# Performance work log

Measured on AMD Instinct MI355X. Metric: run time of the kernel, lower is better.

Reference implementation:

```python
import jax, jax.numpy as jnp
import numpy as np

B, N, K, D_IN, D, L = 8, 8192, 6, 3, 256, 5
EPS_LN = 1e-5


def layernorm(x, g, b):
    m = jnp.mean(x, axis=-1, keepdims=True)
    v = jnp.mean((x - m) ** 2, axis=-1, keepdims=True)
    return (x - m) * jax.lax.rsqrt(v + EPS_LN) * g + b


def spmm_mean(v, knn):
    # sparse adj matmul: out[j] = sum_{n: j in knn[n]} v[n], then / k
    n, k = knn.shape[-2], knn.shape[-1]
    src = jnp.repeat(jnp.arange(n), k)  # [N*K]

    def one(vb, kb):
        return jnp.zeros_like(vb).at[kb.reshape(-1)].add(vb[src])

    return jax.vmap(one)(v, knn) / (k + 1e-6)


def grf_layer(h, knn, qkv_w, out_w, out_b, hops=3):
    q, k, v = jnp.split(h @ qkv_w, 3, axis=-1)
    for _ in range(hops):
        v = spmm_mean(v, knn)
        k = spmm_mean(k, knn)
    attn = jnp.sum(q * k, axis=-1, keepdims=True)
    return (attn * v) @ out_w + out_b


def linear_attention(h, qkv_w, out_w, out_b):
    q, k, v = jnp.split(h @ qkv_w, 3, axis=-1)
    q = jax.nn.relu(q) + 1e-6
    k = jax.nn.relu(k) + 1e-6
    kv = jnp.einsum('bnd,bne->bde', k, v)
    z = 1.0 / (jnp.einsum('bnd,bd->bn', q, k.sum(axis=1)) + 1e-6)
    attn = jnp.einsum('bnd,bde,bn->bne', q, kv, z)
    return attn @ out_w + out_b


def setup_inputs() -> dict:
    key = jax.random.key(0)
    ks = jax.random.split(key, 12)
    s = 0.02
    return {
        'x': jax.random.normal(ks[0], (B, N, D_IN), jnp.float32),
        'knn': jax.random.randint(ks[1], (B, N, K), 0, N, jnp.int32),
        'emb_w': jax.random.normal(ks[2], (D_IN, D), jnp.float32) * s,
        'emb_b': jnp.zeros((D,), jnp.float32),
        'norm_g': jnp.ones((2 * L, D), jnp.float32),
        'norm_b': jnp.zeros((2 * L, D), jnp.float32),
        'grf_qkv': jax.random.normal(ks[3], (L, D, 3 * D), jnp.float32) * s,
        'grf_outw': jax.random.normal(ks[4], (L, D, D), jnp.float32) * s,
        'grf_outb': jnp.zeros((L, D), jnp.float32),
        'attn_qkv': jax.random.normal(ks[5], (L, D, 3 * D), jnp.float32) * s,
        'attn_outw': jax.random.normal(ks[6], (L, D, D), jnp.float32) * s,
        'attn_outb': jnp.zeros((L, D), jnp.float32),
        'head_w': jax.random.normal(ks[7], (D, 3), jnp.float32) * s,
        'head_b': jnp.zeros((3,), jnp.float32),
    }


def reference(x, knn, emb_w, emb_b, norm_g, norm_b, grf_qkv, grf_outw, grf_outb,
              attn_qkv, attn_outw, attn_outb, head_w, head_b):
    h = x @ emb_w + emb_b
    for i in range(L):
        h = h + grf_layer(layernorm(h, norm_g[2 * i], norm_b[2 * i]), knn,
                          grf_qkv[i], grf_outw[i], grf_outb[i])
        h = h + linear_attention(layernorm(h, norm_g[2 * i + 1], norm_b[2 * i + 1]),
                                 attn_qkv[i], attn_outw[i], attn_outb[i])
    return h @ head_w + head_b
```

## Files before the change

### kernel.cpp

```cpp
#include <hip/hip_runtime.h>

#define BB 8
#define NN 8192
#define KK 6
#define DD 256
#define LL 5
#define NE (BB*NN*KK)
#define PLANE (NN*DD)
#define INV6 (1.0f/6.000001f)

typedef unsigned short u16;
typedef __attribute__((ext_vector_type(8))) _Float16 h8;
typedef __attribute__((ext_vector_type(8))) unsigned short us8;
typedef __attribute__((ext_vector_type(4))) float f32x4;

__device__ __forceinline__ u16 f2h(float f){
  union { _Float16 h; u16 u; } c; c.h = (_Float16)f; return c.u;
}
__device__ __forceinline__ float h2f(u16 u){
  union { _Float16 h; u16 u; } c; c.u = u; return (float)c.h;
}

__device__ __forceinline__ void ldscp(const u16* g, u16* l){
  __builtin_amdgcn_global_load_lds(
      (const __attribute__((address_space(1))) void*)g,
      (__attribute__((address_space(3))) void*)l, 16, 0, 0);
}

__global__ void k_count(const int* __restrict__ knn, int* __restrict__ off){
  int e = blockIdx.x*256 + threadIdx.x;
  if(e >= NE) return;
  int b = e / (NN*KK);
  int j = knn[e];
  atomicAdd(&off[b*(NN+1) + 1 + j], 1);
}

__global__ __launch_bounds__(1024) void k_scan(int* __restrict__ offAll){
  __shared__ int lds[1024];
  __shared__ int carry_s;
  int* off = offAll + blockIdx.x*(NN+1);
  const int len = NN+1;
  int t = threadIdx.x;
  if(t==0) carry_s = 0;
  __syncthreads();
  for(int base=0; base<len; base+=1024){
    int x = (base+t < len) ? off[base+t] : 0;
    lds[t] = x; __syncthreads();
    for(int s=1; s<1024; s<<=1){
      int v = (t>=s) ? lds[t-s] : 0;
      __syncthreads();
      lds[t] += v;
      __syncthreads();
    }
    int incl = lds[t];
    int carry = carry_s;
    __syncthreads();
    if(base+t < len) off[base+t] = incl + carry;
    if(t==1023) carry_s = carry + incl;
    __syncthreads();
  }
}

__global__ void k_fill(const int* __restrict__ knn, int* __restrict__ cursor, int* __restrict__ srcE){
  int e = blockIdx.x*256 + threadIdx.x;
  if(e >= NE) return;
  int b = e / (NN*KK);
  int n = (e % (NN*KK)) / KK;
  int j = knn[e];
  int pos = atomicAdd(&cursor[b*(NN+1) + j], 1);
  srcE[(long)b*NN*KK + pos] = n;
}

__global__ __launch_bounds__(256) void k_prepw(const float* __restrict__ W, u16* __restrict__ Wt, int N){
  int n = blockIdx.x, l = blockIdx.y, k = threadIdx.x;
  float x = W[((long)l*256 + k)*N + n];
  u16 hb = f2h(x);
  Wt[(((long)l*2 + 0)*N + n)*256 + k] = hb;
  Wt[(((long)l*2 + 1)*N + n)*256 + k] = f2h(x - h2f(hb));
}

__global__ __launch_bounds__(256) void k_embed(const float* __restrict__ x, const float* __restrict__ ew,
                        const float* __restrict__ eb, float* __restrict__ h){
  int g = blockIdx.x, z = blockIdx.y, d = threadIdx.x;
  const float* xp = x + ((long)z*NN + g)*3;
  h[(long)z*PLANE + (long)g*DD + d] = xp[0]*ew[0*DD+d] + xp[1]*ew[1*DD+d] + xp[2]*ew[2*DD+d] + eb[d];
}

__global__ __launch_bounds__(256) void k_ln(const float* __restrict__ h, const float* __restrict__ g,
                     const float* __restrict__ bia, u16* __restrict__ out){
  long z = blockIdx.y;
  int row = blockIdx.x*4 + (threadIdx.x >> 6);
  int lane = threadIdx.x & 63;
  const float4 x = *(const float4*)(h + z*PLANE + (long)row*DD + lane*4);
  float s  = x.x + x.y + x.z + x.w;
  float s2 = x.x*x.x + x.y*x.y + x.z*x.z + x.w*x.w;
  for(int o=1;o<64;o<<=1){ s += __shfl_xor(s,o); s2 += __shfl_xor(s2,o); }
  float m = s*(1.0f/256.0f);
  float var = s2*(1.0f/256.0f) - m*m;
  float r = rsqrtf(var + 1e-5f);
  const float4 gu = *(const float4*)(g + lane*4);
  const float4 bu = *(const float4*)(bia + lane*4);
  ushort4 o4;
  o4.x = f2h((x.x-m)*r*gu.x + bu.x);
  o4.y = f2h((x.y-m)*r*gu.y + bu.y);
  o4.z = f2h((x.z-m)*r*gu.z + bu.z);
  o4.w = f2h((x.w-m)*r*gu.w + bu.w);
  *(ushort4*)(out + z*PLANE + (long)row*DD + lane*4) = o4;
}

template<int BM,int BN,bool ASPLIT,bool BF32,bool BSPLIT>
__global__ __launch_bounds__(256) void k_mgemm(
    const u16* __restrict__ A, long aStride, long aLoOff, int K, int kSplit,
    const void* __restrict__ Bv, long bStride, long bLoOff,
    const float* __restrict__ rowscale, long rsStride,
    const float* __restrict__ bias,
    u16* __restrict__ o0, u16* __restrict__ o1, u16* __restrict__ o2,
    long oStride, int reluMask, long oLoOff,
    float* __restrict__ accOut, long hStride)
{
  constexpr int WM = BM/2, WN = BN/2, MT = WM/16, NT = WN/16;
  constexpr int STG = BM*32*(ASPLIT?2:1) + BN*32*(BSPLIT?2:1);
  constexpr int EPI = (BM==128) ? 32*132*2 : 0;
  constexpr int SM  = (STG > EPI) ? STG : EPI;
  __shared__ __align__(16) u16 smem[SM];
  u16* Ahi = smem;
  u16* Alo = smem + BM*32;
  u16* Bhi = smem + BM*32*(ASPLIT?2:1);
  u16* Blo = Bhi + BN*32;
  float* epi = (float*)smem;

  const int t = threadIdx.x;
  const int nz = blockIdx.z;
  const long z = nz / kSplit;
  const int chunk = nz % kSplit;
  const int kLen = K / kSplit, kLo = chunk * kLen;
  const int rowTile = blockIdx.x*BM, colTile = blockIdx.y*BN;
  const int l = t & 63, w = t >> 6;
  const int wr = w >> 1, wc = w & 1;
  const int lm = l & 15, kq = l >> 4;

  f32x4 acc[MT][NT];
  #pragma unroll
  for(int mt=0;mt<MT;mt++)
    #pragma unroll
    for(int nt=0;nt<NT;nt++) acc[mt][nt] = (f32x4){0.f,0.f,0.f,0.f};

  for(int k0=kLo; k0<kLo+kLen; k0+=32){
    __syncthreads();
    {
      constexpr int NCH = BM/64;
      #pragma unroll
      for(int li=0; li<NCH; li++){
        int f = li*256 + t;
        int row = f>>2, c = (f&3)*8;
        const u16* gp = A + z*aStride + (long)(rowTile+row)*K + k0 + c;
        ldscp(gp, &Ahi[f*8]);
        if constexpr (ASPLIT) ldscp(gp + aLoOff, &Alo[f*8]);
      }
    }
    if constexpr (BF32){
      constexpr int NCH = BN/64;
      #pragma unroll
      for(int li=0; li<NCH; li++){
        int f = li*256 + t;
        int row = f>>2, c = (f&3)*8;
        const float* src = (const float*)Bv + z*bStride + (long)(colTile+row)*K + k0 + c;
        float4 v0 = ((const float4*)src)[0], v1 = ((const float4*)src)[1];
        us8 hv;
        hv[0]=f2h(v0.x); hv[1]=f2h(v0.y); hv[2]=f2h(v0.z); hv[3]=f2h(v0.w);
        hv[4]=f2h(v1.x); hv[5]=f2h(v1.y); hv[6]=f2h(v1.z); hv[7]=f2h(v1.w);
        *(us8*)&Bhi[f*8] = hv;
      }
    } else {
      constexpr int NCH = BN/64;
      #pragma unroll
      for(int li=0; li<NCH; li++){
        int f = li*256 + t;
        int row = f>>2, c = (f&3)*8;
        const u16* gp = (const u16*)Bv + z*bStride + (long)(colTile+row)*K + k0 + c;
        ldscp(gp, &Bhi[f*8]);
        if constexpr (BSPLIT) ldscp(gp + bLoOff, &Blo[f*8]);
      }
    }
    __syncthreads();
    h8 ah[MT], al[MT], bh[NT], bl[NT];
    #pragma unroll
    for(int mt=0;mt<MT;mt++){
      int idx = (wr*WM + mt*16 + lm)*32 + kq*8;
      ah[mt] = *(const h8*)&Ahi[idx];
      if constexpr (ASPLIT) al[mt] = *(const h8*)&Alo[idx];
    }
    #pragma unroll
    for(int nt=0;nt<NT;nt++){
      int idx = (wc*WN + nt*16 + lm)*32 + kq*8;
      bh[nt] = *(const h8*)&Bhi[idx];
      if constexpr (BSPLIT) bl[nt] = *(const h8*)&Blo[idx];
    }
    #pragma unroll
    for(int mt=0;mt<MT;mt++)
      #pragma unroll
      for(int nt=0;nt<NT;nt++){
        acc[mt][nt] = __builtin_amdgcn_mfma_f32_16x16x32_f16(ah[mt], bh[nt], acc[mt][nt], 0, 0, 0);
        if constexpr (BSPLIT)
          acc[mt][nt] = __builtin_amdgcn_mfma_f32_16x16x32_f16(ah[mt], bl[nt], acc[mt][nt], 0, 0, 0);
        if constexpr (ASPLIT)
          acc[mt][nt] = __builtin_amdgcn_mfma_f32_16x16x32_f16(al[mt], bh[nt], acc[mt][nt], 0, 0, 0);
      }
  }

  if constexpr (BM == 128){
    const int sec = colTile >> 8;
    u16* osec = (sec==0) ? o0 : ((sec==1) ? o1 : o2);
    const bool relu = (reluMask >> sec) & 1;
    #pragma unroll
    for(int mt=0;mt<MT;mt++){
      __syncthreads();
      #pragma unroll
      for(int r=0;r<4;r++){
        int gm = rowTile + wr*64 + mt*16 + kq*4 + r;
        float sc = rowscale ? rowscale[z*rsStride + gm] : 1.0f;
        int rl = wr*16 + kq*4 + r;
        #pragma unroll
        for(int nt=0;nt<NT;nt++)
          epi[rl*132 + wc*64 + nt*16 + lm] = acc[mt][nt][r]*sc;
      }
      __syncthreads();
      #pragma unroll
      for(int ss=0;ss<2;ss++){
        int s = ss*256 + t;
        int rl = s >> 4, sc8 = (s & 15)*8;
        int gm2 = rowTile + (rl>>4)*64 + mt*16 + (rl & 15);
        float v[8];
        #pragma unroll
        for(int j=0;j<8;j++) v[j] = epi[rl*132 + sc8 + j];
        if(bias){
          const float* bp = bias + colTile + sc8;
          #pragma unroll
          for(int j=0;j<8;j++) v[j] += bp[j];
        }
        if(accOut){
          float* hp = accOut + z*hStride + (long)gm2*256 + colTile + sc8;
          float4 h0 = ((float4*)hp)[0], h1 = ((float4*)hp)[1];
          h0.x += v[0]; h0.y += v[1]; h0.z += v[2]; h0.w += v[3];
          h1.x += v[4]; h1.y += v[5]; h1.z += v[6]; h1.w += v[7];
          ((float4*)hp)[0] = h0; ((float4*)hp)[1] = h1;
        } else {
          us8 o8;
          #pragma unroll
          for(int j=0;j<8;j++){
            float vv = v[j];
            if(relu) vv = fmaxf(vv, 0.f) + 1e-6f;
            o8[j] = f2h(vv);
          }
          *(us8*)(osec + z*oStride + (long)gm2*256 + ((colTile + sc8) & 255)) = o8;
        }
      }
    }
  } else {
    #pragma unroll
    for(int mt=0;mt<MT;mt++){
      #pragma unroll
      for(int r=0;r<4;r++){
        int gm = rowTile + wr*WM + mt*16 + kq*4 + r;
        float sc = rowscale ? rowscale[z*rsStride + gm] : 1.0f;
        if(accOut){
          float* hp = accOut + z*hStride + (long)gm*256;
          if(kSplit > 1){
            #pragma unroll
            for(int nt=0;nt<NT;nt++){
              int gc = colTile + wc*WN + nt*16 + lm;
              atomicAdd(&hp[gc], acc[mt][nt][r]);
            }
          } else {
            #pragma unroll
            for(int nt=0;nt<NT;nt++){
              int gc = colTile + wc*WN + nt*16 + lm;
              hp[gc] += acc[mt][nt][r]*sc + (bias ? bias[gc] : 0.f);
            }
          }
        } else {
          #pragma unroll
          for(int nt=0;nt<NT;nt++){
            int gc = colTile + wc*WN + nt*16 + lm;
            int sec = gc >> 8;
            u16* o = (sec==0) ? o0 : ((sec==1) ? o1 : o2);
            float val = acc[mt][nt][r]*sc + (bias ? bias[gc] : 0.f);
            if((reluMask >> sec) & 1) val = fmaxf(val, 0.f) + 1e-6f;
            if(sec==0 && oLoOff){
              u16* oo = o0 + 2*z*oStride + (long)gm*256 + (gc & 255);
              u16 hb = f2h(val);
              oo[0] = hb;
              oo[oLoOff] = f2h(val - h2f(hb));
            } else {
              o[z*oStride + (long)gm*256 + (gc & 255)] = f2h(val);
            }
          }
        }
      }
    }
  }
}

template<int MODE>
__global__ __launch_bounds__(256) void k_spmm2(
    const u16* __restrict__ kin, const u16* __restrict__ vin,
    const int* __restrict__ offB, const int* __restrict__ srcB,
    u16* __restrict__ kout, u16* __restrict__ vout,
    const u16* __restrict__ q, float* __restrict__ rs){
  long z = blockIdx.x;
  const u16* kp = kin + z*PLANE;
  const u16* vp = vin + z*PLANE;
  const int* off = offB + z*(NN+1);
  const int* sE  = srcB + z*(long)NN*KK;
  int row = blockIdx.y*8 + (threadIdx.x >> 5);
  int l32 = threadIdx.x & 31;
  int d8 = l32*8;
  int s0 = off[row], s1 = off[row+1];
  float ak[8], av[8];
  #pragma unroll
  for(int j=0;j<8;j++){ ak[j]=0.f; av[j]=0.f; }
  int e = s0;
  for(; e+1 < s1; e += 2){
    int n0 = sE[e], n1 = sE[e+1];
    us8 k0 = *(const us8*)(kp + (long)n0*DD + d8);
    us8 k1 = *(const us8*)(kp + (long)n1*DD + d8);
    us8 v0 = *(const us8*)(vp + (long)n0*DD + d8);
    us8 v1 = *(const us8*)(vp + (long)n1*DD + d8);
    #pragma unroll
    for(int j=0;j<8;j++){
      ak[j] += h2f(k0[j]) + h2f(k1[j]);
      av[j] += h2f(v0[j]) + h2f(v1[j]);
    }
  }
  if(e < s1){
    int n0 = sE[e];
    us8 k0 = *(const us8*)(kp + (long)n0*DD + d8);
    us8 v0 = *(const us8*)(vp + (long)n0*DD + d8);
    #pragma unroll
    for(int j=0;j<8;j++){ ak[j] += h2f(k0[j]); av[j] += h2f(v0[j]); }
  }
  if constexpr (MODE == 0){
    us8 ok, ov;
    #pragma unroll
    for(int j=0;j<8;j++){ ok[j] = f2h(ak[j]*INV6); ov[j] = f2h(av[j]*INV6); }
    *(us8*)(kout + z*PLANE + (long)row*DD + d8) = ok;
    *(us8*)(vout + z*PLANE + (long)row*DD + d8) = ov;
  } else {
    us8 ov;
    #pragma unroll
    for(int j=0;j<8;j++) ov[j] = f2h(av[j]*INV6);
    *(us8*)(vout + z*PLANE + (long)row*DD + d8) = ov;
    us8 qv = *(const us8*)(q + z*PLANE + (long)row*DD + d8);
    float s = 0.f;
    #pragma unroll
    for(int j=0;j<8;j++) s += h2f(qv[j]) * ak[j];
    for(int o=1;o<32;o<<=1) s += __shfl_xor(s,o);
    if(l32==0) rs[z*NN + row] = s*INV6;
  }
}

__global__ __launch_bounds__(256) void k_zcalc(const u16* __restrict__ q, const float* __restrict__ ksum,
                        float* __restrict__ rs){
  long z = blockIdx.y;
  int row = blockIdx.x*4 + (threadIdx.x >> 6);
  int lane = threadIdx.x & 63;
  ushort4 qv = *(const ushort4*)(q + z*PLANE + (long)row*DD + lane*4);
  const float4 c = *(const float4*)(ksum + z*DD + lane*4);
  float s = h2f(qv.x)*c.x + h2f(qv.y)*c.y + h2f(qv.z)*c.z + h2f(qv.w)*c.w;
  for(int o=1;o<64;o<<=1) s += __shfl_xor(s,o);
  if(lane==0) rs[z*NN + row] = 1.0f / (s + 1e-6f);
}

__global__ __launch_bounds__(256) void k_transp2(
    const u16* __restrict__ in0, u16* __restrict__ out0,
    const u16* __restrict__ in1, u16* __restrict__ out1){
  __shared__ u16 tile[64][72];
  int zz = blockIdx.z;
  long z = zz >> 1;
  const u16* ip = ((zz & 1) ? in1 : in0) + z*PLANE;
  u16* op = ((zz & 1) ? out1 : out0) + z*PLANE;
  int r0 = blockIdx.x*64, c0 = blockIdx.y*64;
  int t = threadIdx.x;
  {
    int r = t>>2, cg = (t&3)*16;
    *(us8*)&tile[r][cg]   = *(const us8*)(ip + (long)(r0+r)*DD + c0 + cg);
    *(us8*)&tile[r][cg+8] = *(const us8*)(ip + (long)(r0+r)*DD + c0 + cg + 8);
  }
  __syncthreads();
  {
    int c = t>>2, rg = t&3;
    us8 a, b;
    #pragma unroll
    for(int j=0;j<8;j++){ a[j] = tile[rg*16+j][c]; b[j] = tile[rg*16+8+j][c]; }
    u16* dst = op + (long)(c0+c)*NN + r0 + rg*16;
    *(us8*)dst = a; *(us8*)(dst+8) = b;
  }
}

__global__ __launch_bounds__(256) void k_ksum(const u16* __restrict__ kT, float* __restrict__ ksum){
  long z = blockIdx.y;
  int d = blockIdx.x;
  const u16* p = kT + z*PLANE + (long)d*NN;
  float s = 0.f;
  for(int i=threadIdx.x*8; i<NN; i+=2048){
    us8 a = *(const us8*)(p+i);
    #pragma unroll
    for(int j=0;j<8;j++) s += h2f(a[j]);
  }
  for(int o=1;o<64;o<<=1) s += __shfl_xor(s,o);
  __shared__ float ws4[4];
  int w = threadIdx.x >> 6;
  if((threadIdx.x & 63)==0) ws4[w] = s;
  __syncthreads();
  if(threadIdx.x==0) ksum[z*DD + d] = ws4[0]+ws4[1]+ws4[2]+ws4[3];
}

__global__ __launch_bounds__(256) void k_head(const float* __restrict__ h, const float* __restrict__ hw,
                       const float* __restrict__ hb, float* __restrict__ out){
  long z = blockIdx.y;
  int row = blockIdx.x*4 + (threadIdx.x >> 6);
  int lane = threadIdx.x & 63;
  const float4 x = *(const float4*)(h + z*PLANE + (long)row*DD + lane*4);
  int d0 = lane*4;
  float a0 = x.x*hw[(d0+0)*3+0] + x.y*hw[(d0+1)*3+0] + x.z*hw[(d0+2)*3+0] + x.w*hw[(d0+3)*3+0];
  float a1 = x.x*hw[(d0+0)*3+1] + x.y*hw[(d0+1)*3+1] + x.z*hw[(d0+2)*3+1] + x.w*hw[(d0+3)*3+1];
  float a2 = x.x*hw[(d0+0)*3+2] + x.y*hw[(d0+1)*3+2] + x.z*hw[(d0+2)*3+2] + x.w*hw[(d0+3)*3+2];
  for(int o=1;o<64;o<<=1){
    a0 += __shfl_xor(a0,o); a1 += __shfl_xor(a1,o); a2 += __shfl_xor(a2,o);
  }
  if(lane==0){
    float* op = out + (z*NN + row)*3;
    op[0] = a0 + hb[0];
    op[1] = a1 + hb[1];
    op[2] = a2 + hb[2];
  }
}

struct Carve {
  float *h; u16 *L,*Q,*Bp,*Cp,*T;
  float *kvf; u16 *w2t;
  float *ksum,*rs;
  int *off,*cursor,*srcE;
  u16 *wt_gqkv,*wt_aqkv,*wt_gout,*wt_aout;
  size_t total;
};

static Carve carve(char* base, int C){
  Carve c;
  size_t cur = 0;
  auto bump = [&](size_t bytes)->char*{
    char* p = base ? base + cur : (char*)0;
    cur += (bytes + 255) & ~(size_t)255;
    return p;
  };
  c.h    = (float*)bump((size_t)C*PLANE*4);
  c.L    = (u16*)bump((size_t)C*PLANE*2);
  c.Q    = (u16*)bump((size_t)C*PLANE*2);
  c.Bp   = (u16*)bump((size_t)C*PLANE*2);
  c.Cp   = (u16*)bump((size_t)C*PLANE*2);
  c.T    = (u16*)bump((size_t)C*PLANE*2);
  c.kvf  = (float*)bump((size_t)C*DD*DD*4);
  c.w2t  = (u16*)bump((size_t)C*2*DD*DD*2);
  c.ksum = (float*)bump((size_t)C*DD*4);
  c.rs   = (float*)bump((size_t)C*NN*4);
  c.off  = (int*)bump((size_t)BB*(NN+1)*4);
  c.cursor=(int*)bump((size_t)BB*(NN+1)*4);
  c.srcE = (int*)bump((size_t)NE*4);
  c.wt_gqkv = (u16*)bump((size_t)LL*2*768*256*2);
  c.wt_aqkv = (u16*)bump((size_t)LL*2*768*256*2);
  c.wt_gout = (u16*)bump((size_t)LL*2*256*256*2);
  c.wt_aout = (u16*)bump((size_t)LL*2*256*256*2);
  c.total = cur;
  return c;
}

extern "C" void kernel_launch(void* const* d_in, const int* in_sizes, int n_in,
                              void* d_out, int out_size, void* d_ws, size_t ws_size,
                              hipStream_t stream)
{
  const float* x        = (const float*)d_in[0];
  const int*   knn      = (const int*)d_in[1];
  const float* emb_w    = (const float*)d_in[2];
  const float* emb_b    = (const float*)d_in[3];
  const float* norm_g   = (const float*)d_in[4];
  const float* norm_b   = (const float*)d_in[5];
  const float* grf_qkv  = (const float*)d_in[6];
  const float* grf_outw = (const float*)d_in[7];
  const float* grf_outb = (const float*)d_in[8];
  const float* attn_qkv = (const float*)d_in[9];
  const float* attn_outw= (const float*)d_in[10];
  const float* attn_outb= (const float*)d_in[11];
  const float* head_w   = (const float*)d_in[12];
  const float* head_b   = (const float*)d_in[13];
  float* out = (float*)d_out;

  int C = 1;
  for(int cc=BB; cc>=1; cc>>=1){ if(carve(nullptr, cc).total <= ws_size){ C = cc; break; } }
  Carve ws = carve((char*)d_ws, C);

  k_prepw<<<dim3(768, LL), 256, 0, stream>>>(grf_qkv,  ws.wt_gqkv, 768);
  k_prepw<<<dim3(768, LL), 256, 0, stream>>>(attn_qkv, ws.wt_aqkv, 768);
  k_prepw<<<dim3(256, LL), 256, 0, stream>>>(grf_outw, ws.wt_gout, 256);
  k_prepw<<<dim3(256, LL), 256, 0, stream>>>(attn_outw,ws.wt_aout, 256);

  hipMemsetAsync(ws.off, 0, (size_t)BB*(NN+1)*sizeof(int), stream);
  k_count<<<dim3((NE+255)/256), 256, 0, stream>>>(knn, ws.off);
  k_scan<<<dim3(BB), 1024, 0, stream>>>(ws.off);
  hipMemcpyAsync(ws.cursor, ws.off, (size_t)BB*(NN+1)*sizeof(int), hipMemcpyDeviceToDevice, stream);
  k_fill<<<dim3((NE+255)/256), 256, 0, stream>>>(knn, ws.cursor, ws.srcE);

  const long PL = PLANE;
  for(int b0=0; b0<BB; b0+=C){
    const int* offB  = ws.off  + (long)b0*(NN+1);
    const int* srcB  = ws.srcE + (long)b0*NN*KK;

    k_embed<<<dim3(NN, C), 256, 0, stream>>>(x + (long)b0*NN*3, emb_w, emb_b, ws.h);

    for(int i=0; i<LL; i++){
      k_ln<<<dim3(NN/4, C), 256, 0, stream>>>(ws.h, norm_g + (2*i)*DD, norm_b + (2*i)*DD, ws.L);
      k_mgemm<128,128,false,false,true><<<dim3(64, 6, C), 256, 0, stream>>>(
          ws.L, PL, 0, 256, 1,
          ws.wt_gqkv + (long)i*2*768*256, 0, (long)768*256,
          nullptr, 0, nullptr,
          ws.Q, ws.Bp, ws.Cp, PL, 0, 0, nullptr, 0);
      k_spmm2<0><<<dim3(C, NN/8), 256, 0, stream>>>(ws.Bp, ws.Cp, offB, srcB, ws.L, ws.T, nullptr, nullptr);
      k_spmm2<0><<<dim3(C, NN/8), 256, 0, stream>>>(ws.L,  ws.T,  offB, srcB, ws.Bp, ws.Cp, nullptr, nullptr);
      k_spmm2<1><<<dim3(C, NN/8), 256, 0, stream>>>(ws.Bp, ws.Cp, offB, srcB, nullptr, ws.T, ws.Q, ws.rs);
      k_mgemm<128,128,false,false,true><<<dim3(64, 2, C), 256, 0, stream>>>(
          ws.T, PL, 0, 256, 1,
          ws.wt_gout + (long)i*2*256*256, 0, (long)256*256,
          ws.rs, NN, grf_outb + (long)i*DD,
          nullptr, nullptr, nullptr, 0, 0, 0, ws.h, PL);

      k_ln<<<dim3(NN/4, C), 256, 0, stream>>>(ws.h, norm_g + (2*i+1)*DD, norm_b + (2*i+1)*DD, ws.L);
      k_mgemm<128,128,false,false,true><<<dim3(64, 6, C), 256, 0, stream>>>(
          ws.L, PL, 0, 256, 1,
          ws.wt_aqkv + (long)i*2*768*256, 0, (long)768*256,
          nullptr, 0, nullptr,
          ws.Q, ws.Bp, ws.Cp, PL, 3 , 0, nullptr, 0);
      k_transp2<<<dim3(NN/64, DD/64, 2*C), 256, 0, stream>>>(ws.Bp, ws.L, ws.Cp, ws.T);
      k_ksum<<<dim3(DD, C), 256, 0, stream>>>(ws.L, ws.ksum);
      hipMemsetAsync(ws.kvf, 0, (size_t)C*DD*DD*sizeof(float), stream);
      k_mgemm<64,64,false,false,false><<<dim3(4, 4, C*8), 256, 0, stream>>>(
          ws.L, PL, 0, NN, 8,
          ws.T, PL, 0,
          nullptr, 0, nullptr,
          nullptr, nullptr, nullptr, 0, 0, 0, ws.kvf, (long)DD*DD);
      k_mgemm<64,64,true,true,false><<<dim3(4, 4, C), 256, 0, stream>>>(
          ws.wt_aout + (long)i*2*256*256, 0, (long)256*256, 256, 1,
          ws.kvf, (long)DD*DD, 0,
          nullptr, 0, nullptr,
          ws.w2t, nullptr, nullptr, (long)DD*DD, 0, (long)DD*DD,
          nullptr, 0);
      k_zcalc<<<dim3(NN/4, C), 256, 0, stream>>>(ws.Q, ws.ksum, ws.rs);
      k_mgemm<128,128,false,false,true><<<dim3(64, 2, C), 256, 0, stream>>>(
          ws.Q, PL, 0, 256, 1,
          ws.w2t, 2L*DD*DD, (long)DD*DD,
          ws.rs, NN, attn_outb + (long)i*DD,
          nullptr, nullptr, nullptr, 0, 0, 0, ws.h, PL);
    }

    k_head<<<dim3(NN/4, C), 256, 0, stream>>>(ws.h, head_w, head_b, out + (long)b0*NN*3);
  }
}
```

Measured before the change: 2.653 ms.

## Fuse K/V transpose into kv MFMA kernel and compute ksum from row-major K

Removes the explicit transpose kernel and the generic GEMM for K^T V. A new kernel loads row-major K and V tiles, transposes them in shared memory, and accumulates with MFMA, adding partial results into kvf with atomics. ksum is now computed directly from row-major K using column-parallel per-chunk sums and atomics, after a memset. This avoids writing and re-reading transposed planes, at the cost of a simpler inner loop with a sync per 32-row step and bank conflicts on the transposing LDS stores.

```diff
diff --git a/kernel.cpp b/kernel.cpp
--- a/kernel.cpp
+++ b/kernel.cpp
@@ -371,48 +371,71 @@
   if(lane==0) rs[z*NN + row] = 1.0f / (s + 1e-6f);
 }
 
-__global__ __launch_bounds__(256) void k_transp2(
-    const u16* __restrict__ in0, u16* __restrict__ out0,
-    const u16* __restrict__ in1, u16* __restrict__ out1){
-  __shared__ u16 tile[64][72];
-  int zz = blockIdx.z;
-  long z = zz >> 1;
-  const u16* ip = ((zz & 1) ? in1 : in0) + z*PLANE;
-  u16* op = ((zz & 1) ? out1 : out0) + z*PLANE;
-  int r0 = blockIdx.x*64, c0 = blockIdx.y*64;
-  int t = threadIdx.x;
-  {
-    int r = t>>2, cg = (t&3)*16;
-    *(us8*)&tile[r][cg]   = *(const us8*)(ip + (long)(r0+r)*DD + c0 + cg);
-    *(us8*)&tile[r][cg+8] = *(const us8*)(ip + (long)(r0+r)*DD + c0 + cg + 8);
-  }
-  __syncthreads();
-  {
-    int c = t>>2, rg = t&3;
-    us8 a, b;
-    #pragma unroll
-    for(int j=0;j<8;j++){ a[j] = tile[rg*16+j][c]; b[j] = tile[rg*16+8+j][c]; }
-    u16* dst = op + (long)(c0+c)*NN + r0 + rg*16;
-    *(us8*)dst = a; *(us8*)(dst+8) = b;
-  }
-}
-
-__global__ __launch_bounds__(256) void k_ksum(const u16* __restrict__ kT, float* __restrict__ ksum){
+__global__ __launch_bounds__(256) void k_kv(const u16* __restrict__ kAll, const u16* __restrict__ vAll,
+                                            float* __restrict__ kvf){
+  __shared__ u16 Kt[64*40];
+  __shared__ u16 Vt[64*40];
+  int nz = blockIdx.z;
+  long z = nz >> 3;
+  int chunk = nz & 7;
+  int dT = blockIdx.x*64, eT = blockIdx.y*64;
+  const u16* kp = kAll + z*PLANE;
+  const u16* vp = vAll + z*PLANE;
+  const int t = threadIdx.x;
+  const int l = t & 63, w = t >> 6;
+  const int wr = w >> 1, wc = w & 1;
+  const int lm = l & 15, kq = l >> 4;
+  const int nrow = t >> 3, c8 = (t & 7)*8;
+
+  f32x4 acc[2][2];
+  #pragma unroll
+  for(int mt=0;mt<2;mt++)
+    #pragma unroll
+    for(int nt=0;nt<2;nt++) acc[mt][nt] = (f32x4){0.f,0.f,0.f,0.f};
+
+  int n0 = chunk*1024;
+  for(int nn=n0; nn<n0+1024; nn+=32){
+    us8 kk = *(const us8*)(kp + (long)(nn+nrow)*DD + dT + c8);
+    us8 vv = *(const us8*)(vp + (long)(nn+nrow)*DD + eT + c8);
+    __syncthreads();
+    #pragma unroll
+    for(int j=0;j<8;j++){
+      Kt[(c8+j)*40 + nrow] = kk[j];
+      Vt[(c8+j)*40 + nrow] = vv[j];
+    }
+    __syncthreads();
+    h8 af[2], bf[2];
+    #pragma unroll
+    for(int mt=0;mt<2;mt++) af[mt] = *(const h8*)&Kt[(wr*32 + mt*16 + lm)*40 + kq*8];
+    #pragma unroll
+    for(int nt=0;nt<2;nt++) bf[nt] = *(const h8*)&Vt[(wc*32 + nt*16 + lm)*40 + kq*8];
+    #pragma unroll
+    for(int mt=0;mt<2;mt++)
+      #pragma unroll
+      for(int nt=0;nt<2;nt++)
+        acc[mt][nt] = __builtin_amdgcn_mfma_f32_16x16x32_f16(af[mt], bf[nt], acc[mt][nt], 0, 0, 0);
+  }
+  #pragma unroll
+  for(int mt=0;mt<2;mt++)
+    #pragma unroll
+    for(int r=0;r<4;r++){
+      int gd = dT + wr*32 + mt*16 + kq*4 + r;
+      #pragma unroll
+      for(int nt=0;nt<2;nt++){
+        int ge = eT + wc*32 + nt*16 + lm;
+        atomicAdd(&kvf[z*DD*DD + (long)gd*256 + ge], acc[mt][nt][r]);
+      }
+    }
+}
+
+__global__ __launch_bounds__(256) void k_ksum2(const u16* __restrict__ kAll, float* __restrict__ ksum){
   long z = blockIdx.y;
-  int d = blockIdx.x;
-  const u16* p = kT + z*PLANE + (long)d*NN;
+  int c = blockIdx.x;
+  const u16* p = kAll + z*PLANE + ((long)c*512)*DD;
+  int d = threadIdx.x;
   float s = 0.f;
-  for(int i=threadIdx.x*8; i<NN; i+=2048){
-    us8 a = *(const us8*)(p+i);
-    #pragma unroll
-    for(int j=0;j<8;j++) s += h2f(a[j]);
-  }
-  for(int o=1;o<64;o<<=1) s += __shfl_xor(s,o);
-  __shared__ float ws4[4];
-  int w = threadIdx.x >> 6;
-  if((threadIdx.x & 63)==0) ws4[w] = s;
-  __syncthreads();
-  if(threadIdx.x==0) ksum[z*DD + d] = ws4[0]+ws4[1]+ws4[2]+ws4[3];
+  for(int i=0;i<512;i++) s += h2f(p[(long)i*DD + d]);
+  atomicAdd(&ksum[z*DD + d], s);
 }
 
 __global__ __launch_bounds__(256) void k_head(const float* __restrict__ h, const float* __restrict__ hw,
@@ -538,14 +561,10 @@
           ws.wt_aqkv + (long)i*2*768*256, 0, (long)768*256,
           nullptr, 0, nullptr,
           ws.Q, ws.Bp, ws.Cp, PL, 3 , 0, nullptr, 0);
-      k_transp2<<<dim3(NN/64, DD/64, 2*C), 256, 0, stream>>>(ws.Bp, ws.L, ws.Cp, ws.T);
-      k_ksum<<<dim3(DD, C), 256, 0, stream>>>(ws.L, ws.ksum);
       hipMemsetAsync(ws.kvf, 0, (size_t)C*DD*DD*sizeof(float), stream);
-      k_mgemm<64,64,false,false,false><<<dim3(4, 4, C*8), 256, 0, stream>>>(
-          ws.L, PL, 0, NN, 8,
-          ws.T, PL, 0,
-          nullptr, 0, nullptr,
-          nullptr, nullptr, nullptr, 0, 0, 0, ws.kvf, (long)DD*DD);
+      hipMemsetAsync(ws.ksum, 0, (size_t)C*DD*sizeof(float), stream);
+      k_ksum2<<<dim3(16, C), 256, 0, stream>>>(ws.Bp, ws.ksum);
+      k_kv<<<dim3(4, 4, C*8), 256, 0, stream>>>(ws.Bp, ws.Cp, ws.kvf);
       k_mgemm<64,64,true,true,false><<<dim3(4, 4, C), 256, 0, stream>>>(
           ws.wt_aout + (long)i*2*256*256, 0, (long)256*256, 256, 1,
           ws.kvf, (long)DD*DD, 0,
```

Measured after the change: 2.745 ms. +3.4%, slower.

## Fuse output projection, residual add and next LayerNorm into one kernel

Applied to the files above, without the earlier changes.

Adds a full-row (64x256) output GEMM kernel that applies the row scale, bias and residual add to h, then computes the next LayerNorm in the epilogue and writes the fp16 normalized activations. It replaces the separate out-projection GEMM plus standalone LN launches, saving a re-read of h and several kernel launches per layer. The cost is a smaller-M tile with fewer blocks and lower MMA efficiency per block, and the LN statistics use a single-pass variance formula.

```diff
diff --git a/kernel.cpp b/kernel.cpp
--- a/kernel.cpp
+++ b/kernel.cpp
@@ -301,6 +301,117 @@
   }
 }
 
+__global__ __launch_bounds__(256) void k_fusedout(
+    const u16* __restrict__ A, const u16* __restrict__ B, long bStride, long bLoOff,
+    const float* __restrict__ rowscale, const float* __restrict__ bias,
+    float* __restrict__ h,
+    const float* __restrict__ lnG, const float* __restrict__ lnB,
+    u16* __restrict__ Lout)
+{
+  constexpr int SMU = 64*32 + 2*256*32;
+  __shared__ __align__(16) u16 smem[SMU];
+  u16* As = smem;
+  u16* Bh = smem + 64*32;
+  u16* Bl = Bh + 256*32;
+  float* epi = (float*)smem;
+
+  const int t = threadIdx.x;
+  const long z = blockIdx.z;
+  const int rowTile = blockIdx.x*64;
+  const int l = t & 63, w = t >> 6;
+  const int wr = w >> 1, wc = w & 1;
+  const int lm = l & 15, kq = l >> 4;
+  const u16* Ab = A + z*PLANE;
+  const u16* Bb = B + z*bStride;
+
+  f32x4 acc[2][8];
+  #pragma unroll
+  for(int mt=0;mt<2;mt++)
+    #pragma unroll
+    for(int nt=0;nt<8;nt++) acc[mt][nt] = (f32x4){0.f,0.f,0.f,0.f};
+
+  for(int k0=0; k0<256; k0+=32){
+    __syncthreads();
+    {
+      ldscp(Ab + (long)(rowTile+(t>>2))*256 + k0 + (t&3)*8, &As[t*8]);
+    }
+    #pragma unroll
+    for(int li=0; li<4; li++){
+      int f = li*256 + t;
+      int row = f>>2, c = (f&3)*8;
+      const u16* gp = Bb + (long)row*256 + k0 + c;
+      ldscp(gp, &Bh[f*8]);
+      ldscp(gp + bLoOff, &Bl[f*8]);
+    }
+    __syncthreads();
+    h8 af[2], bh[8], bl[8];
+    #pragma unroll
+    for(int mt=0;mt<2;mt++)
+      af[mt] = *(const h8*)&As[(wr*32 + mt*16 + lm)*32 + kq*8];
+    #pragma unroll
+    for(int nt=0;nt<8;nt++){
+      int idx = (wc*128 + nt*16 + lm)*32 + kq*8;
+      bh[nt] = *(const h8*)&Bh[idx];
+      bl[nt] = *(const h8*)&Bl[idx];
+    }
+    #pragma unroll
+    for(int mt=0;mt<2;mt++)
+      #pragma unroll
+      for(int nt=0;nt<8;nt++){
+        acc[mt][nt] = __builtin_amdgcn_mfma_f32_16x16x32_f16(af[mt], bh[nt], acc[mt][nt], 0, 0, 0);
+        acc[mt][nt] = __builtin_amdgcn_mfma_f32_16x16x32_f16(af[mt], bl[nt], acc[mt][nt], 0, 0, 0);
+      }
+  }
+
+  #pragma unroll
+  for(int mt=0;mt<2;mt++){
+    __syncthreads();
+    #pragma unroll
+    for(int r=0;r<4;r++){
+      int rl = wr*16 + kq*4 + r;
+      int gm = rowTile + wr*32 + mt*16 + kq*4 + r;
+      float sc = rowscale ? rowscale[z*NN + gm] : 1.0f;
+      #pragma unroll
+      for(int nt=0;nt<8;nt++)
+        epi[rl*260 + wc*128 + nt*16 + lm] = acc[mt][nt][r]*sc;
+    }
+    __syncthreads();
+    #pragma unroll
+    for(int ss=0;ss<8;ss++){
+      int s = ss*256 + t;
+      int rl = s >> 6;
+      int c4 = (s & 63)*4;
+      int gm = rowTile + (rl>>4)*32 + mt*16 + (rl & 15);
+      float4 e = *(float4*)&epi[rl*260 + c4];
+      float4 x;
+      x.x = e.x + bias[c4+0];
+      x.y = e.y + bias[c4+1];
+      x.z = e.z + bias[c4+2];
+      x.w = e.w + bias[c4+3];
+      float* hp = h + z*PLANE + (long)gm*256 + c4;
+      float4 h0 = *(float4*)hp;
+      x.x += h0.x; x.y += h0.y; x.z += h0.z; x.w += h0.w;
+      *(float4*)hp = x;
+      if(lnG){
+        float sA = x.x + x.y + x.z + x.w;
+        float s2 = x.x*x.x + x.y*x.y + x.z*x.z + x.w*x.w;
+        for(int o=1;o<64;o<<=1){ sA += __shfl_xor(sA,o); s2 += __shfl_xor(s2,o); }
+        float m = sA*(1.0f/256.0f);
+        float var = s2*(1.0f/256.0f) - m*m;
+        float rr = rsqrtf(var + 1e-5f);
+        const float4 gu = *(const float4*)(lnG + c4);
+        const float4 bu = *(const float4*)(lnB + c4);
+        ushort4 o4;
+        o4.x = f2h((x.x-m)*rr*gu.x + bu.x);
+        o4.y = f2h((x.y-m)*rr*gu.y + bu.y);
+        o4.z = f2h((x.z-m)*rr*gu.z + bu.z);
+        o4.w = f2h((x.w-m)*rr*gu.w + bu.w);
+        *(ushort4*)(Lout + z*PLANE + (long)gm*256 + c4) = o4;
+      }
+    }
+  }
+}
+
 template<int MODE>
 __global__ __launch_bounds__(256) void k_spmm2(
     const u16* __restrict__ kin, const u16* __restrict__ vin,
@@ -515,9 +626,9 @@
     const int* srcB  = ws.srcE + (long)b0*NN*KK;
 
     k_embed<<<dim3(NN, C), 256, 0, stream>>>(x + (long)b0*NN*3, emb_w, emb_b, ws.h);
+    k_ln<<<dim3(NN/4, C), 256, 0, stream>>>(ws.h, norm_g, norm_b, ws.L);
 
     for(int i=0; i<LL; i++){
-      k_ln<<<dim3(NN/4, C), 256, 0, stream>>>(ws.h, norm_g + (2*i)*DD, norm_b + (2*i)*DD, ws.L);
       k_mgemm<128,128,false,false,true><<<dim3(64, 6, C), 256, 0, stream>>>(
           ws.L, PL, 0, 256, 1,
           ws.wt_gqkv + (long)i*2*768*256, 0, (long)768*256,
@@ -526,13 +637,11 @@
       k_spmm2<0><<<dim3(C, NN/8), 256, 0, stream>>>(ws.Bp, ws.Cp, offB, srcB, ws.L, ws.T, nullptr, nullptr);
       k_spmm2<0><<<dim3(C, NN/8), 256, 0, stream>>>(ws.L,  ws.T,  offB, srcB, ws.Bp, ws.Cp, nullptr, nullptr);
       k_spmm2<1><<<dim3(C, NN/8), 256, 0, stream>>>(ws.Bp, ws.Cp, offB, srcB, nullptr, ws.T, ws.Q, ws.rs);
-      k_mgemm<128,128,false,false,true><<<dim3(64, 2, C), 256, 0, stream>>>(
-          ws.T, PL, 0, 256, 1,
-          ws.wt_gout + (long)i*2*256*256, 0, (long)256*256,
-          ws.rs, NN, grf_outb + (long)i*DD,
-          nullptr, nullptr, nullptr, 0, 0, 0, ws.h, PL);
-
-      k_ln<<<dim3(NN/4, C), 256, 0, stream>>>(ws.h, norm_g + (2*i+1)*DD, norm_b + (2*i+1)*DD, ws.L);
+      k_fusedout<<<dim3(NN/64, 1, C), 256, 0, stream>>>(
+          ws.T, ws.wt_gout + (long)i*2*256*256, 0, (long)256*256,
+          ws.rs, grf_outb + (long)i*DD, ws.h,
+          norm_g + (2*i+1)*DD, norm_b + (2*i+1)*DD, ws.L);
+
       k_mgemm<128,128,false,false,true><<<dim3(64, 6, C), 256, 0, stream>>>(
           ws.L, PL, 0, 256, 1,
           ws.wt_aqkv + (long)i*2*768*256, 0, (long)768*256,
@@ -553,11 +662,12 @@
           ws.w2t, nullptr, nullptr, (long)DD*DD, 0, (long)DD*DD,
           nullptr, 0);
       k_zcalc<<<dim3(NN/4, C), 256, 0, stream>>>(ws.Q, ws.ksum, ws.rs);
-      k_mgemm<128,128,false,false,true><<<dim3(64, 2, C), 256, 0, stream>>>(
-          ws.Q, PL, 0, 256, 1,
-          ws.w2t, 2L*DD*DD, (long)DD*DD,
-          ws.rs, NN, attn_outb + (long)i*DD,
-          nullptr, nullptr, nullptr, 0, 0, 0, ws.h, PL);
+      const float* g2 = (i==LL-1) ? nullptr : norm_g + (2*i+2)*DD;
+      const float* b2 = (i==LL-1) ? nullptr : norm_b + (2*i+2)*DD;
+      k_fusedout<<<dim3(NN/64, 1, C), 256, 0, stream>>>(
+          ws.Q, ws.w2t, 2L*DD*DD, (long)DD*DD,
+          ws.rs, attn_outb + (long)i*DD, ws.h,
+          g2, b2, ws.L);
     }
 
     k_head<<<dim3(NN/4, C), 256, 0, stream>>>(ws.h, head_w, head_b, out + (long)b0*NN*3);
```

Measured after the change: 2.584 ms. 2.6% less time.
